# Performance work log

Measured on AMD Instinct MI355X. Metric: run time of the kernel, lower is better.

## Reference

```python
import jax, jax.numpy as jnp
import numpy as np

B, C_IN, H, W = 4, 64, 384, 384
C_OUT, KER, R = 64, 3, 4
N = B * H * W


def _conv(x, w):
    # NCHW conv, stride 1, SAME padding (ker//2 for odd kernels)
    return jax.lax.conv_general_dilated(
        x, w, window_strides=(1, 1), padding='SAME',
        dimension_numbers=('NCHW', 'OIHW', 'NCHW'))


def setup_inputs() -> dict:
    key = jax.random.key(0)
    kx, kp, k1, k2, k3 = jax.random.split(key, 5)
    x = jax.random.normal(kx, (B, C_IN, H, W), dtype=jnp.float32)
    # disjoint partition of all b*h*w pixel indices
    perm = jax.random.permutation(kp, N)
    mask_idx = perm[: N // 2].astype(jnp.int32)
    inv_mask_idx = perm[N // 2:].astype(jnp.int32)
    # weights, init per the torch module: std = sqrt(2 / (out_channels * kH*kW))
    std_high = np.sqrt(2.0 / (C_OUT * KER * KER)).astype(np.float32)
    std_low1 = np.sqrt(2.0 / ((C_OUT // R) * KER * KER)).astype(np.float32)
    std_low2 = np.sqrt(2.0 / (C_OUT * 1 * 1)).astype(np.float32)
    high_w = jax.random.normal(k1, (C_OUT, C_IN, KER, KER), dtype=jnp.float32) * std_high
    low1_w = jax.random.normal(k2, (C_OUT // R, C_IN, KER, KER), dtype=jnp.float32) * std_low1
    low2_w = jax.random.normal(k3, (C_OUT, C_OUT // R, 1, 1), dtype=jnp.float32) * std_low2
    return {"x": x, "high_w": high_w, "low1_w": low1_w, "low2_w": low2_w,
            "mask_idx": mask_idx, "inv_mask_idx": inv_mask_idx}


def reference(x, high_w, low1_w, low2_w, mask_idx, inv_mask_idx):
    # eval_forward: per-pixel routed conv (no bias on either path).
    # Pixels in mask_idx get the full 3x3 conv; pixels in inv_mask_idx get the
    # low-rank bottleneck path (3x3 conv to C/r, then 1x1 conv back to C).
    b, c, h, w = x.shape
    n = b * h * w
    high = _conv(x, high_w)                     # (b, cout, h, w)
    low = _conv(_conv(x, low1_w), low2_w)       # (b, cout, h, w)
    # flatten to pixel-major order matching torch's b*h*w flattening
    hf = high.transpose(0, 2, 3, 1).reshape(n, -1)  # (n, cout)
    lf = low.transpose(0, 2, 3, 1).reshape(n, -1)
    is_high = jnp.zeros((n,), dtype=bool).at[mask_idx].set(True)
    yf = jnp.where(is_high[:, None], hf, lf)
    return yf.reshape(b, h, w, -1).transpose(0, 3, 1, 2)
```

## Files before the change

### kernel.cpp

```cpp
#include <hip/hip_runtime.h>
#include <hip/hip_bf16.h>
#include <stdint.h>

typedef __attribute__((ext_vector_type(8))) short  short8;
typedef __attribute__((ext_vector_type(4))) float  float4_t;
typedef __attribute__((ext_vector_type(4))) int    int4_t;

constexpr int BB = 4, CIN = 64, COUT = 64, HH = 384, WW = 384;
constexpr int HWc  = HH * WW;
constexpr int NPIX = BB * HWc;
constexpr int WP   = 386;
constexpr int TR = 12, TC = 32;
constexpr int SR = TR + 2, SC = TC + 2;

__device__ __forceinline__ unsigned short f2bf(float f) {
    unsigned u = __builtin_bit_cast(unsigned, f);
    unsigned r = u + 0x7FFFu + ((u >> 16) & 1u);
    return (unsigned short)(r >> 16);
}

__global__ void k_flags(const int* __restrict__ mi, const int* __restrict__ ii,
                        unsigned char* __restrict__ flags, int half) {
    int i = blockIdx.x * blockDim.x + threadIdx.x;
    if (i < half) { flags[mi[i]] = 1; flags[ii[i]] = 0; }
}

__global__ void k_zb(unsigned short* __restrict__ xt) {
    int i = blockIdx.x * 256 + threadIdx.x;
    if (i >= 4 * 98560) return;
    int b = i / 98560, j = i % 98560;
    size_t off;
    if (j < 2 * 386 * 64) {
        int yt  = (j >= 386 * 64) ? 385 : 0;
        int jj  = j % (386 * 64);
        int col = jj >> 6, cin = jj & 63;
        off = (((size_t)b * WP + yt) * WP + col) * 64 + cin;
    } else {
        int j2  = j - 2 * 386 * 64;
        int xtc = (j2 >= 384 * 64) ? 385 : 0;
        int jj  = j2 % (384 * 64);
        int row = 1 + (jj >> 6), cin = jj & 63;
        off = (((size_t)b * WP + row) * WP + xtc) * 64 + cin;
    }
    xt[off] = 0;
}

__global__ __launch_bounds__(256) void k_xpose(const float* __restrict__ x,
                                               unsigned short* __restrict__ xt) {
    __shared__ float tile[64][65];
    const int xt0 = blockIdx.x * 64;
    const int y   = blockIdx.y;
    const int b   = blockIdx.z;
    const int t   = threadIdx.x;
    {
        int col = t & 63, ci0 = t >> 6;
        const float* xp = x + (size_t)(b * 64) * HWc + y * WW + xt0 + col;
#pragma unroll
        for (int i = 0; i < 16; i++) {
            int cin = i * 4 + ci0;
            tile[cin][col] = xp[(size_t)cin * HWc];
        }
    }
    __syncthreads();
    {
        int c2 = (t & 31) * 2, colw = t >> 5;
        unsigned short* op = xt + (((size_t)b * WP + (y + 1)) * WP + (xt0 + 1)) * 64;
#pragma unroll
        for (int i = 0; i < 8; i++) {
            int cc = colw + i * 8;
            unsigned lo = f2bf(tile[c2][cc]);
            unsigned hi = f2bf(tile[c2 + 1][cc]);
            *(unsigned*)(op + (size_t)cc * 64 + c2) = lo | (hi << 16);
        }
    }
}

__global__ void k_wpack(const float* __restrict__ hw_, const float* __restrict__ l1w,
                        const float* __restrict__ l2w,
                        unsigned short* __restrict__ Wp, unsigned short* __restrict__ Ap2) {
    int i = blockIdx.x * 256 + threadIdx.x;
    if (i < 18 * 5 * 64) {
        int lane = i & 63, tile = (i >> 6) % 5, chunk = i / 320;
        int tap = chunk >> 1, h = chunk & 1, ky = tap / 3, kx = tap % 3;
        int m = lane & 15, quad = lane >> 4;
        for (int j = 0; j < 8; j++) {
            int cin = h * 32 + quad * 8 + j;
            float wv;
            if (tile < 4) { int co = tile * 16 + m; wv = hw_[((co * 64 + cin) * 3 + ky) * 3 + kx]; }
            else          { wv = l1w[((m * 64 + cin) * 3 + ky) * 3 + kx]; }
            Wp[(size_t)i * 8 + j] = f2bf(wv);
        }
    }
    if (i < 4 * 64) {
        int lane = i & 63, tile = i >> 6;
        int m = lane & 15, quad = lane >> 4;
        for (int j = 0; j < 8; j++) {
            unsigned short v = 0;
            if (j < 4) { int c = quad * 4 + j; v = f2bf(l2w[(tile * 16 + m) * 16 + c]); }
            Ap2[(size_t)i * 8 + j] = v;
        }
    }
}

__global__ __launch_bounds__(256, 2) void k_main(
    const unsigned short* __restrict__ xt,
    const unsigned short* __restrict__ Wp,
    const unsigned short* __restrict__ Ap2,
    const unsigned char* __restrict__ flags,
    float* __restrict__ out)
{
    __shared__ __align__(16) unsigned short X[SR * SC * 64];

    const int tid = threadIdx.x;
    const int x0  = blockIdx.x * TC;
    const int y0  = blockIdx.y * TR;
    const int b   = blockIdx.z;

    const unsigned short* xbase = xt + (((size_t)b * WP + y0) * WP + x0) * 64;
    for (int s = tid; s < SR * SC * 8; s += 256) {
        int c8 = s & 7;
        int xh = (s >> 3) % SC;
        int rh = s / (SC * 8);
        int4_t v = *(const int4_t*)(xbase + ((size_t)rh * WP + xh) * 64 + c8 * 8);
        int blk = c8 ^ (xh & 7);
        *(int4_t*)&X[(rh * SC + xh) * 64 + blk * 8] = v;
    }
    __syncthreads();

    const int lane = tid & 63;
    const int w    = tid >> 6;
    const int n16  = lane & 15;
    const int quad = lane >> 4;

    float4_t acc[5][6];
#pragma unroll
    for (int t = 0; t < 5; t++)
#pragma unroll
        for (int f = 0; f < 6; f++) acc[t][f] = (float4_t)0.0f;

    const int4_t* wp4 = (const int4_t*)Wp;
    short8 a_cur[5], a_nxt[5];
#pragma unroll
    for (int t = 0; t < 5; t++)
        a_cur[t] = __builtin_bit_cast(short8, wp4[t * 64 + lane]);

#pragma unroll 1
    for (int chunk = 0; chunk < 18; chunk++) {
        if (chunk < 17) {
#pragma unroll
            for (int t = 0; t < 5; t++)
                a_nxt[t] = __builtin_bit_cast(short8, wp4[((chunk + 1) * 5 + t) * 64 + lane]);
        }
        const int tap = chunk >> 1, h = chunk & 1;
        const int ky = tap / 3, kx = tap % 3;
        short8 bf[6];
#pragma unroll
        for (int f = 0; f < 6; f++) {
            int idx = w * 6 + f;
            int r = idx >> 1, ch = idx & 1;
            int xh  = ch * 16 + n16 + kx;
            int blk = (h * 4 + quad) ^ (xh & 7);
            bf[f] = __builtin_bit_cast(short8,
                    *(const int4_t*)&X[((r + ky) * SC + xh) * 64 + blk * 8]);
        }
#pragma unroll
        for (int f = 0; f < 6; f++)
#pragma unroll
            for (int t = 0; t < 5; t++)
                acc[t][f] = __builtin_amdgcn_mfma_f32_16x16x32_bf16(a_cur[t], bf[f], acc[t][f], 0, 0, 0);
#pragma unroll
        for (int t = 0; t < 5; t++) a_cur[t] = a_nxt[t];
    }

    short8 a2[4];
    const int4_t* ap4 = (const int4_t*)Ap2;
#pragma unroll
    for (int t = 0; t < 4; t++)
        a2[t] = __builtin_bit_cast(short8, ap4[t * 64 + lane]);

#pragma unroll
    for (int f = 0; f < 6; f++) {
        int idx = w * 6 + f;
        int r = idx >> 1, ch = idx & 1;
        float4_t m4 = acc[4][f];
        short8 bfrag;
#pragma unroll
        for (int j = 0; j < 8; j++)
            bfrag[j] = (j < 4) ? (short)f2bf(m4[j]) : (short)0;

        int gy = y0 + r, gx = x0 + ch * 16 + n16;
        bool hiF = flags[b * HWc + gy * WW + gx] != 0;
        float* ob = out + (size_t)b * COUT * HWc + gy * WW + gx;
#pragma unroll
        for (int t = 0; t < 4; t++) {
            float4_t low = __builtin_amdgcn_mfma_f32_16x16x32_bf16(a2[t], bfrag, (float4_t)0.0f, 0, 0, 0);
            float4_t hi = acc[t][f];
#pragma unroll
            for (int i = 0; i < 4; i++) {
                int co = t * 16 + quad * 4 + i;
                ob[(size_t)co * HWc] = hiF ? hi[i] : low[i];
            }
        }
    }
}

extern "C" void kernel_launch(void* const* d_in, const int* in_sizes, int n_in,
                              void* d_out, int out_size, void* d_ws, size_t ws_size,
                              hipStream_t stream) {
    const float* x   = (const float*)d_in[0];
    const float* hw_ = (const float*)d_in[1];
    const float* l1w = (const float*)d_in[2];
    const float* l2w = (const float*)d_in[3];
    const int*   mi  = (const int*)d_in[4];
    const int*   ii  = (const int*)d_in[5];
    float*       out = (float*)d_out;

    unsigned short* xt    = (unsigned short*)d_ws;
    size_t off = (size_t)4 * WP * WP * 64 * 2;
    unsigned char*  flags = (unsigned char*)d_ws + off;  off += NPIX;
    off = (off + 15) & ~(size_t)15;
    unsigned short* Wp    = (unsigned short*)((char*)d_ws + off); off += 18 * 5 * 64 * 8 * 2;
    unsigned short* Ap2   = (unsigned short*)((char*)d_ws + off);

    const int half = NPIX / 2;
    k_flags<<<(half + 255) / 256, 256, 0, stream>>>(mi, ii, flags, half);
    k_zb<<<(4 * 98560 + 255) / 256, 256, 0, stream>>>(xt);
    k_xpose<<<dim3(WW / 64, HH, BB), 256, 0, stream>>>(x, xt);
    k_wpack<<<(18 * 5 * 64 + 255) / 256, 256, 0, stream>>>(hw_, l1w, l2w, Wp, Ap2);
    k_main<<<dim3(WW / TC, HH / TR, BB), 256, 0, stream>>>(xt, Wp, Ap2, flags, out);
}
```

Measured before the change: 345.3 us.

## Fuse NCHW-to-bf16 transpose and padding into main conv kernel tile load

```diff
diff --git a/kernel.cpp b/kernel.cpp
--- a/kernel.cpp
+++ b/kernel.cpp
@@ -9,9 +9,9 @@
 constexpr int BB = 4, CIN = 64, COUT = 64, HH = 384, WW = 384;
 constexpr int HWc  = HH * WW;
 constexpr int NPIX = BB * HWc;
-constexpr int WP   = 386;
 constexpr int TR = 12, TC = 32;
 constexpr int SR = TR + 2, SC = TC + 2;
+constexpr int NGRP = SR * SC * 8;
 
 __device__ __forceinline__ unsigned short f2bf(float f) {
     unsigned u = __builtin_bit_cast(unsigned, f);
@@ -23,56 +23,6 @@
                         unsigned char* __restrict__ flags, int half) {
     int i = blockIdx.x * blockDim.x + threadIdx.x;
     if (i < half) { flags[mi[i]] = 1; flags[ii[i]] = 0; }
-}
-
-__global__ void k_zb(unsigned short* __restrict__ xt) {
-    int i = blockIdx.x * 256 + threadIdx.x;
-    if (i >= 4 * 98560) return;
-    int b = i / 98560, j = i % 98560;
-    size_t off;
-    if (j < 2 * 386 * 64) {
-        int yt  = (j >= 386 * 64) ? 385 : 0;
-        int jj  = j % (386 * 64);
-        int col = jj >> 6, cin = jj & 63;
-        off = (((size_t)b * WP + yt) * WP + col) * 64 + cin;
-    } else {
-        int j2  = j - 2 * 386 * 64;
-        int xtc = (j2 >= 384 * 64) ? 385 : 0;
-        int jj  = j2 % (384 * 64);
-        int row = 1 + (jj >> 6), cin = jj & 63;
-        off = (((size_t)b * WP + row) * WP + xtc) * 64 + cin;
-    }
-    xt[off] = 0;
-}
-
-__global__ __launch_bounds__(256) void k_xpose(const float* __restrict__ x,
-                                               unsigned short* __restrict__ xt) {
-    __shared__ float tile[64][65];
-    const int xt0 = blockIdx.x * 64;
-    const int y   = blockIdx.y;
-    const int b   = blockIdx.z;
-    const int t   = threadIdx.x;
-    {
-        int col = t & 63, ci0 = t >> 6;
-        const float* xp = x + (size_t)(b * 64) * HWc + y * WW + xt0 + col;
-#pragma unroll
-        for (int i = 0; i < 16; i++) {
-            int cin = i * 4 + ci0;
-            tile[cin][col] = xp[(size_t)cin * HWc];
-        }
-    }
-    __syncthreads();
-    {
-        int c2 = (t & 31) * 2, colw = t >> 5;
-        unsigned short* op = xt + (((size_t)b * WP + (y + 1)) * WP + (xt0 + 1)) * 64;
-#pragma unroll
-        for (int i = 0; i < 8; i++) {
-            int cc = colw + i * 8;
-            unsigned lo = f2bf(tile[c2][cc]);
-            unsigned hi = f2bf(tile[c2 + 1][cc]);
-            *(unsigned*)(op + (size_t)cc * 64 + c2) = lo | (hi << 16);
-        }
-    }
 }
 
 __global__ void k_wpack(const float* __restrict__ hw_, const float* __restrict__ l1w,
@@ -103,7 +53,7 @@
 }
 
 __global__ __launch_bounds__(256, 2) void k_main(
-    const unsigned short* __restrict__ xt,
+    const float* __restrict__ x,
     const unsigned short* __restrict__ Wp,
     const unsigned short* __restrict__ Ap2,
     const unsigned char* __restrict__ flags,
@@ -116,14 +66,28 @@
     const int y0  = blockIdx.y * TR;
     const int b   = blockIdx.z;
 
-    const unsigned short* xbase = xt + (((size_t)b * WP + y0) * WP + x0) * 64;
-    for (int s = tid; s < SR * SC * 8; s += 256) {
-        int c8 = s & 7;
-        int xh = (s >> 3) % SC;
-        int rh = s / (SC * 8);
-        int4_t v = *(const int4_t*)(xbase + ((size_t)rh * WP + xh) * 64 + c8 * 8);
-        int blk = c8 ^ (xh & 7);
-        *(int4_t*)&X[(rh * SC + xh) * 64 + blk * 8] = v;
+    const float* xb = x + (size_t)b * CIN * HWc;
+#pragma unroll 1
+    for (int s = tid; s < NGRP; s += 256) {
+        int q   = s / (SR * SC);
+        int p   = s - q * (SR * SC);
+        int row = p / SC;
+        int col = p - row * SC;
+        int gy  = y0 + row - 1;
+        int gx  = x0 + col - 1;
+        bool ok = ((unsigned)gy < (unsigned)HH) && ((unsigned)gx < (unsigned)WW);
+        int off = ok ? (gy * WW + gx) : 0;
+        const float* xp = xb + (size_t)(q * 8) * HWc + off;
+        unsigned pk[4];
+#pragma unroll
+        for (int jj = 0; jj < 4; jj++) {
+            float f0 = xp[(size_t)(2 * jj)     * HWc];
+            float f1 = xp[(size_t)(2 * jj + 1) * HWc];
+            if (!ok) { f0 = 0.f; f1 = 0.f; }
+            pk[jj] = (unsigned)f2bf(f0) | ((unsigned)f2bf(f1) << 16);
+        }
+        int blk = q ^ (col & 7);
+        *(int4_t*)&X[p * 64 + blk * 8] = *(int4_t*)pk;
     }
     __syncthreads();
 
@@ -215,17 +179,13 @@
     const int*   ii  = (const int*)d_in[5];
     float*       out = (float*)d_out;
 
-    unsigned short* xt    = (unsigned short*)d_ws;
-    size_t off = (size_t)4 * WP * WP * 64 * 2;
-    unsigned char*  flags = (unsigned char*)d_ws + off;  off += NPIX;
-    off = (off + 15) & ~(size_t)15;
+    unsigned char*  flags = (unsigned char*)d_ws;
+    size_t off = (NPIX + 15) & ~(size_t)15;
     unsigned short* Wp    = (unsigned short*)((char*)d_ws + off); off += 18 * 5 * 64 * 8 * 2;
     unsigned short* Ap2   = (unsigned short*)((char*)d_ws + off);
 
     const int half = NPIX / 2;
     k_flags<<<(half + 255) / 256, 256, 0, stream>>>(mi, ii, flags, half);
-    k_zb<<<(4 * 98560 + 255) / 256, 256, 0, stream>>>(xt);
-    k_xpose<<<dim3(WW / 64, HH, BB), 256, 0, stream>>>(x, xt);
     k_wpack<<<(18 * 5 * 64 + 255) / 256, 256, 0, stream>>>(hw_, l1w, l2w, Wp, Ap2);
-    k_main<<<dim3(WW / TC, HH / TR, BB), 256, 0, stream>>>(xt, Wp, Ap2, flags, out);
+    k_main<<<dim3(WW / TC, HH / TR, BB), 256, 0, stream>>>(x, Wp, Ap2, flags, out);
 }
```

Measured after the change: 344.7 us. No clear change (-0.2%).
